# Kernel optimization log

Measured on AMD Instinct MI355X. Metric: run time of the kernel, lower is better.

Reference implementation:

```python
import jax, jax.numpy as jnp
import numpy as np

D, H, L, E, K, FF, VIS, NC, NT = 1024, 8, 4, 4, 2, 2048, 1536, 4, 4
HD = D // H


def layer_norm(x, g, b, eps=1e-5):
    m = x.mean(-1, keepdims=True)
    v = ((x - m) ** 2).mean(-1, keepdims=True)
    return (x - m) / jnp.sqrt(v + eps) * g + b


def sinusoidal_pos(seq_len):
    pos = jnp.arange(seq_len, dtype=jnp.float32)[:, None]
    div = jnp.exp(jnp.arange(0, D, 2, dtype=jnp.float32) * (-jnp.log(10000.0) / D))
    pe = jnp.zeros((seq_len, D), dtype=jnp.float32)
    pe = pe.at[:, 0::2].set(jnp.sin(pos * div))
    pe = pe.at[:, 1::2].set(jnp.cos(pos * div))
    return pe


def mha(x, wi, bi, wo, bo):
    # wi: [D, 3D] (pre-transposed), wo: [D, D]
    B, S, _ = x.shape
    qkv = x @ wi + bi
    q, k, v = jnp.split(qkv, 3, axis=-1)
    split = lambda t: t.reshape(B, S, H, HD).transpose(0, 2, 1, 3)
    q, k, v = split(q), split(k), split(v)
    scores = jnp.einsum('bhqd,bhkd->bhqk', q, k) / jnp.sqrt(jnp.float32(HD))
    a = jax.nn.softmax(scores, axis=-1)
    o = jnp.einsum('bhqk,bhkd->bhqd', a, v).transpose(0, 2, 1, 3).reshape(B, S, D)
    return o @ wo + bo


def moe(x_flat, rw, rb, w1, b1, w2, b2):
    # x_flat: [N, D]; rw: [D, E]; w1: [E, D, FF]; w2: [E, FF, D]
    logits = x_flat @ rw + rb                      # [N, E]
    topv, topi = jax.lax.top_k(logits, K)          # [N, K]
    probs = jax.nn.softmax(topv, axis=-1)          # softmax over the top-k logits
    onehot = jax.nn.one_hot(topi, E, dtype=x_flat.dtype)      # [N, K, E]
    combine = jnp.einsum('nk,nke->ne', probs, onehot)         # [N, E]
    h = jax.nn.relu(jnp.einsum('nd,edf->enf', x_flat, w1) + b1[:, None, :])  # [E, N, FF]
    o = jnp.einsum('enf,efd->end', h, w2) + b2[:, None, :]                   # [E, N, D]
    return jnp.einsum('ne,end->nd', combine, o)


def setup_inputs() -> dict:
    key = jax.random.key(0)
    ks = iter(jax.random.split(key, 32))
    s = 0.02
    n = lambda shape: jax.random.normal(next(ks), shape, dtype=jnp.float32) * s
    inp = {
        'vis_feat': jax.random.normal(next(ks), (64, 128, VIS), dtype=jnp.float32),
        'proj_w': n((VIS, D)), 'proj_b': jnp.zeros((D,), jnp.float32),
        'in_proj_w': n((L, D, 3 * D)), 'in_proj_b': jnp.zeros((L, 3 * D), jnp.float32),
        'out_proj_w': n((L, D, D)), 'out_proj_b': jnp.zeros((L, D), jnp.float32),
        'ln1_g': jnp.ones((L, D), jnp.float32), 'ln1_b': jnp.zeros((L, D), jnp.float32),
        'ln2_g': jnp.ones((L, D), jnp.float32), 'ln2_b': jnp.zeros((L, D), jnp.float32),
        'router_w': n((L, D, E)), 'router_b': jnp.zeros((L, E), jnp.float32),
        'ew1': n((L, E, D, FF)), 'eb1': jnp.zeros((L, E, FF), jnp.float32),
        'ew2': n((L, E, FF, D)), 'eb2': jnp.zeros((L, E, D), jnp.float32),
        'attn_w': n((D, 1)), 'attn_b': jnp.zeros((1,), jnp.float32),
        'heads_w': n((NT, D, NC)), 'heads_b': jnp.zeros((NT, NC), jnp.float32),
    }
    return inp


def reference(vis_feat, proj_w, proj_b, in_proj_w, in_proj_b, out_proj_w, out_proj_b,
              ln1_g, ln1_b, ln2_g, ln2_b, router_w, router_b, ew1, eb1, ew2, eb2,
              attn_w, attn_b, heads_w, heads_b):
    B, S, _ = vis_feat.shape
    x = vis_feat @ proj_w + proj_b            # projection to d_model=1024
    x = x + sinusoidal_pos(S)[None]           # positional encoding
    for l in range(L):                         # 4 MoE transformer layers
        x = layer_norm(x + mha(x, in_proj_w[l], in_proj_b[l], out_proj_w[l], out_proj_b[l]),
                       ln1_g[l], ln1_b[l])
        moe_out = moe(x.reshape(B * S, D), router_w[l], router_b[l],
                      ew1[l], eb1[l], ew2[l], eb2[l]).reshape(B, S, D)
        x = layer_norm(x + moe_out, ln2_g[l], ln2_b[l])
    # attention pooling over time, then 4 task heads
    scores = jax.nn.softmax(x @ attn_w + attn_b, axis=1)   # [B, S, 1]
    pooled = jnp.sum(scores * x, axis=1)                   # [B, D]
    logits = jnp.einsum('bd,tdc->tbc', pooled, heads_w) + heads_b[:, None, :]  # [4, B, 4]
    return logits
```

## Files before the change

kernel.cpp:

```cpp
#include <hip/hip_runtime.h>
#include <hip/hip_bf16.h>

typedef unsigned short u16;
typedef unsigned int u32;
using short8 = __attribute__((ext_vector_type(8))) short;
using f32x4  = __attribute__((ext_vector_type(4))) float;

__device__ __forceinline__ u16 f2bu(float f) {
  u32 u = __builtin_bit_cast(u32, f);
  u32 r = u + 0x7fffu + ((u >> 16) & 1u);
  return (u16)(r >> 16);
}
__device__ __forceinline__ float bu2f(u16 u) {
  u32 x = ((u32)u) << 16;
  return __builtin_bit_cast(float, x);
}
__device__ __forceinline__ float waveRedSum(float v) {
  #pragma unroll
  for (int off = 32; off > 0; off >>= 1) v += __shfl_xor(v, off, 64);
  return v;
}
__device__ __forceinline__ void gload16(const void* g, void* l) {
  __builtin_amdgcn_global_load_lds((const __attribute__((address_space(1))) u32*)g,
                                   (__attribute__((address_space(3))) u32*)l, 16, 0, 0);
}

template<int MODE>
__global__ __launch_bounds__(256) void gemm_bt(
    const u16* __restrict__ A, const u16* __restrict__ Bt, const float* __restrict__ bias,
    float* __restrict__ Cf, u16* __restrict__ Cb, u16* __restrict__ M0, u16* __restrict__ M1,
    const int* __restrict__ tok, const float* __restrict__ prob, const int* __restrict__ slot,
    const int* __restrict__ poff, const int* __restrict__ cnts,
    int N, int K)
{
  const int gx = gridDim.x;
  const int nwg = gx * gridDim.y;
  int lid = blockIdx.y * gx + blockIdx.x;
  lid = (lid & 7) * (nwg >> 3) + (lid >> 3);
  const int brow = (lid / gx) << 7, bcol = (lid % gx) << 7;

  int e = 0, rowEnd = 0;
  const u16* Bw = Bt;
  const float* bw = bias;
  if constexpr (MODE >= 2) {
    if (brow >= poff[4]) return;
    #pragma unroll
    for (int q = 1; q < 4; ++q) if (brow >= poff[q]) e = q;
    rowEnd = poff[e] + cnts[e];
    Bw = Bt + (size_t)e * N * K;
    bw = bias + e * N;
  }

  __shared__ __align__(16) u16 As[128 * 64];
  __shared__ __align__(16) u16 Bs[128 * 64];
  const int tid = threadIdx.x;
  const int wave = tid >> 6, lane = tid & 63;
  const int wr = wave >> 1, wc = wave & 1;
  const int r = lane & 15, kg = lane >> 4;

  f32x4 acc[4][4];
  #pragma unroll
  for (int m = 0; m < 4; ++m)
    #pragma unroll
    for (int n = 0; n < 4; ++n) acc[m][n] = f32x4{0.f, 0.f, 0.f, 0.f};

  const u16* aSrc[4];
  const u16* bSrc[4];
  const u16* Bb = Bw + (size_t)bcol * K;
  #pragma unroll
  for (int q = 0; q < 4; ++q) {
    const int cid = (q << 8) + (wave << 6) + lane;
    const int row = cid >> 3, c = cid & 7;
    const int scol = (c ^ (row & 7)) << 3;
    size_t ar;
    if constexpr (MODE == 2) {
      const int g = brow + row;
      ar = (size_t)tok[(g < rowEnd) ? g : poff[e]];
    } else {
      ar = (size_t)(brow + row);
    }
    aSrc[q] = A + ar * K + scol;
    bSrc[q] = Bb + (size_t)row * K + scol;
  }
  const int swz0 = (kg ^ (r & 7)) << 3;
  const int swz1 = ((4 + kg) ^ (r & 7)) << 3;

  for (int k0 = 0; k0 < K; k0 += 64) {
    __syncthreads();
    #pragma unroll
    for (int q = 0; q < 4; ++q) {
      gload16(aSrc[q] + k0, &As[(((q << 8) + (wave << 6))) << 3]);
      gload16(bSrc[q] + k0, &Bs[(((q << 8) + (wave << 6))) << 3]);
    }
    __syncthreads();
    #pragma unroll
    for (int ks = 0; ks < 2; ++ks) {
      const int swz = ks ? swz1 : swz0;
      short8 a[4], b[4];
      #pragma unroll
      for (int m = 0; m < 4; ++m)
        a[m] = *(const short8*)&As[(((wr << 6) + (m << 4) + r) << 6) + swz];
      #pragma unroll
      for (int n = 0; n < 4; ++n)
        b[n] = *(const short8*)&Bs[(((wc << 6) + (n << 4) + r) << 6) + swz];
      #pragma unroll
      for (int m = 0; m < 4; ++m)
        #pragma unroll
        for (int n = 0; n < 4; ++n)
          acc[m][n] = __builtin_amdgcn_mfma_f32_16x16x32_bf16(a[m], b[n], acc[m][n], 0, 0, 0);
    }
  }

  if constexpr (MODE == 3) {
    #pragma unroll
    for (int m = 0; m < 4; ++m) {
      #pragma unroll
      for (int i4 = 0; i4 < 4; ++i4) {
        const int row = brow + (wr << 6) + (m << 4) + (kg << 2) + i4;
        if (row < rowEnd) {
          const int t = tok[row];
          const float pp = prob[row];
          u16* dst = slot[row] ? M1 : M0;
          #pragma unroll
          for (int n = 0; n < 4; ++n) {
            const int col = bcol + (wc << 6) + (n << 4) + r;
            dst[(size_t)t * N + col] = f2bu((acc[m][n][i4] + bw[col]) * pp);
          }
        }
      }
    }
  } else {
    #pragma unroll
    for (int m = 0; m < 4; ++m) {
      #pragma unroll
      for (int n = 0; n < 4; ++n) {
        const int col = bcol + (wc << 6) + (n << 4) + r;
        const float bv = bw[col];
        #pragma unroll
        for (int i4 = 0; i4 < 4; ++i4) {
          const int row = brow + (wr << 6) + (m << 4) + (kg << 2) + i4;
          const float v = acc[m][n][i4] + bv;
          const size_t off = (size_t)row * N + col;
          if constexpr (MODE == 0) Cf[off] = v;
          else if constexpr (MODE == 1) Cb[off] = f2bu(v);
          else Cb[off] = f2bu(fmaxf(v, 0.f));
        }
      }
    }
  }
}

__device__ __forceinline__ void tconv_tile(const float* __restrict__ s, u16* __restrict__ d,
                                           int K, int N, int n0, int k0)
{
  __shared__ float t[32][33];
  const int x = threadIdx.x, y = threadIdx.y;
  #pragma unroll
  for (int j = 0; j < 4; ++j) t[y + 8 * j][x] = s[(size_t)(k0 + y + 8 * j) * N + n0 + x];
  __syncthreads();
  #pragma unroll
  for (int j = 0; j < 4; ++j) d[(size_t)(n0 + y + 8 * j) * K + k0 + x] = f2bu(t[x][y + 8 * j]);
}

__global__ __launch_bounds__(256) void tconv_kernel(const float* __restrict__ src, u16* __restrict__ dst,
                                                    int K, int N)
{
  tconv_tile(src, dst, K, N, blockIdx.x << 5, blockIdx.y << 5);
}

__global__ __launch_bounds__(256) void tconv4_kernel(
    const float* __restrict__ wqkv_s, const float* __restrict__ wout_s,
    const float* __restrict__ we1_s, const float* __restrict__ we2_s,
    u16* __restrict__ wqkv_d, u16* __restrict__ wout_d,
    u16* __restrict__ we1_d, u16* __restrict__ we2_d)
{
  const int bid = blockIdx.x;
  if (bid < 3072) {
    tconv_tile(wqkv_s, wqkv_d, 1024, 3072, (bid % 96) << 5, (bid / 96) << 5);
  } else if (bid < 4096) {
    const int b2 = bid - 3072;
    tconv_tile(wout_s, wout_d, 1024, 1024, (b2 % 32) << 5, (b2 / 32) << 5);
  } else if (bid < 12288) {
    const int b2 = bid - 4096;
    const int ee = b2 >> 11, rr = b2 & 2047;
    tconv_tile(we1_s + (size_t)ee * 2048 * 1024, we1_d + (size_t)ee * 2048 * 1024,
               1024, 2048, (rr % 64) << 5, (rr / 64) << 5);
  } else {
    const int b2 = bid - 12288;
    const int ee = b2 >> 11, rr = b2 & 2047;
    tconv_tile(we2_s + (size_t)ee * 1024 * 2048, we2_d + (size_t)ee * 1024 * 2048,
               2048, 1024, (rr % 32) << 5, (rr / 32) << 5);
  }
}

__global__ __launch_bounds__(256) void conv_kernel(const float* __restrict__ in, u16* __restrict__ out)
{
  const size_t i = ((size_t)blockIdx.x * 256 + threadIdx.x) * 4;
  float4 v = *(const float4*)(in + i);
  *(ushort4*)(out + i) = make_ushort4(f2bu(v.x), f2bu(v.y), f2bu(v.z), f2bu(v.w));
}

__global__ __launch_bounds__(256) void pe_kernel(float* __restrict__ X, u16* __restrict__ Xb)
{
  const int idx = blockIdx.x * 256 + threadIdx.x;
  const int d = idx & 1023;
  const int s = (idx >> 10) & 127;
  const float de = (float)(d & ~1);
  const float ang = (float)s * expf(de * (-9.210340371976184f / 1024.f));
  const float pe = (d & 1) ? cosf(ang) : sinf(ang);
  const float v = X[idx] + pe;
  X[idx] = v;
  Xb[idx] = f2bu(v);
}

__global__ __launch_bounds__(256) void ln_kernel(const float* __restrict__ Xi, const u16* __restrict__ R,
    const float* __restrict__ g, const float* __restrict__ be,
    const float* __restrict__ rw, const float* __restrict__ rb,
    float* __restrict__ Xo, u16* __restrict__ Xbo,
    int* __restrict__ choice, float* __restrict__ prob2)
{
  const int token = blockIdx.x;
  const size_t base = (size_t)token << 10;
  const int tid = threadIdx.x;
  float vals[4]; float s = 0.f, s2 = 0.f;
  #pragma unroll
  for (int j = 0; j < 4; ++j) {
    const int d = tid + (j << 8);
    const float v = Xi[base + d] + bu2f(R[base + d]);
    vals[j] = v; s += v; s2 += v * v;
  }
  s = waveRedSum(s); s2 = waveRedSum(s2);
  __shared__ float rs[4], rs2[4];
  __shared__ float rl[4][4];
  const int wave = tid >> 6, lane = tid & 63;
  if (lane == 0) { rs[wave] = s; rs2[wave] = s2; }
  __syncthreads();
  s = rs[0] + rs[1] + rs[2] + rs[3];
  s2 = rs2[0] + rs2[1] + rs2[2] + rs2[3];
  const float mean = s * (1.f / 1024.f);
  const float var = s2 * (1.f / 1024.f) - mean * mean;
  const float inv = rsqrtf(var + 1e-5f);
  float l0 = 0.f, l1 = 0.f, l2 = 0.f, l3 = 0.f;
  #pragma unroll
  for (int j = 0; j < 4; ++j) {
    const int d = tid + (j << 8);
    const float y = (vals[j] - mean) * inv * g[d] + be[d];
    Xo[base + d] = y;
    Xbo[base + d] = f2bu(y);
    const float4 w = *(const float4*)(rw + ((size_t)d << 2));
    l0 += y * w.x; l1 += y * w.y; l2 += y * w.z; l3 += y * w.w;
  }
  l0 = waveRedSum(l0); l1 = waveRedSum(l1); l2 = waveRedSum(l2); l3 = waveRedSum(l3);
  if (lane == 0) { rl[wave][0] = l0; rl[wave][1] = l1; rl[wave][2] = l2; rl[wave][3] = l3; }
  __syncthreads();
  if (tid == 0) {
    float v[4];
    #pragma unroll
    for (int q = 0; q < 4; ++q)
      v[q] = rl[0][q] + rl[1][q] + rl[2][q] + rl[3][q] + rb[q];
    int i1 = 0;
    for (int q = 1; q < 4; ++q) if (v[q] > v[i1]) i1 = q;
    int i2 = (i1 == 0) ? 1 : 0;
    for (int q = 0; q < 4; ++q) if (q != i1 && v[q] > v[i2]) i2 = q;
    const float p2 = __expf(v[i2] - v[i1]);
    const float is = 1.f / (1.f + p2);
    choice[token] = i1 | (i2 << 8);
    prob2[token * 2]     = is;
    prob2[token * 2 + 1] = p2 * is;
  }
}

__global__ __launch_bounds__(256) void ln2_kernel(const float* __restrict__ Xi,
    const u16* __restrict__ R0, const u16* __restrict__ R1,
    const float* __restrict__ g, const float* __restrict__ be,
    float* __restrict__ Xo, u16* __restrict__ Xbo,
    const float* __restrict__ aw, const float* __restrict__ ab, float* __restrict__ S)
{
  const int token = blockIdx.x;
  const size_t base = (size_t)token << 10;
  const int tid = threadIdx.x;
  float vals[4]; float s = 0.f, s2 = 0.f;
  #pragma unroll
  for (int j = 0; j < 4; ++j) {
    const int d = tid + (j << 8);
    const float v = Xi[base + d] + (bu2f(R0[base + d]) + bu2f(R1[base + d]));
    vals[j] = v; s += v; s2 += v * v;
  }
  s = waveRedSum(s); s2 = waveRedSum(s2);
  __shared__ float rs[4], rs2[4];
  __shared__ float rsc[4];
  const int wave = tid >> 6, lane = tid & 63;
  if (lane == 0) { rs[wave] = s; rs2[wave] = s2; }
  __syncthreads();
  s = rs[0] + rs[1] + rs[2] + rs[3];
  s2 = rs2[0] + rs2[1] + rs2[2] + rs2[3];
  const float mean = s * (1.f / 1024.f);
  const float var = s2 * (1.f / 1024.f) - mean * mean;
  const float inv = rsqrtf(var + 1e-5f);
  float sc = 0.f;
  #pragma unroll
  for (int j = 0; j < 4; ++j) {
    const int d = tid + (j << 8);
    const float y = (vals[j] - mean) * inv * g[d] + be[d];
    Xo[base + d] = y;
    Xbo[base + d] = f2bu(y);
    if (aw) sc += y * aw[d];
  }
  if (aw) {
    sc = waveRedSum(sc);
    if (lane == 0) rsc[wave] = sc;
    __syncthreads();
    if (tid == 0) S[token] = rsc[0] + rsc[1] + rsc[2] + rsc[3] + ab[0];
  }
}

#define LDW 136
__global__ __launch_bounds__(256) void attn_mfma_kernel(const u16* __restrict__ QKVb, u16* __restrict__ ATTb)
{
  __shared__ __align__(16) u16 Kb[128 * LDW];
  __shared__ __align__(16) u16 Vt[128 * LDW];
  u16* Pb = Kb;
  const int b = blockIdx.x >> 3, h = blockIdx.x & 7;
  const int tid = threadIdx.x;
  const int wave = tid >> 6, lane = tid & 63;
  const int r = lane & 15, kg = lane >> 4;
  const u16* base = QKVb + (size_t)b * 128 * 3072 + h * 128;

  for (int i = tid; i < 128 * 16; i += 256) {
    const int row = i >> 4, c8 = (i & 15) << 3;
    *(short8*)&Kb[row * LDW + c8] = *(const short8*)(base + (size_t)row * 3072 + 1024 + c8);
  }
  for (int i = tid; i < 128 * 128; i += 256) {
    const int d = i & 127, key = i >> 7;
    Vt[d * LDW + key] = base[(size_t)key * 3072 + 2048 + d];
  }

  short8 a[2][4];
  #pragma unroll
  for (int m = 0; m < 2; ++m) {
    const int row = wave * 32 + m * 16 + r;
    const u16* qp = base + (size_t)row * 3072;
    #pragma unroll
    for (int ks = 0; ks < 4; ++ks)
      a[m][ks] = *(const short8*)(qp + ks * 32 + kg * 8);
  }
  __syncthreads();

  f32x4 acc[2][8];
  #pragma unroll
  for (int m = 0; m < 2; ++m)
    #pragma unroll
    for (int n = 0; n < 8; ++n) acc[m][n] = f32x4{0.f, 0.f, 0.f, 0.f};
  #pragma unroll
  for (int n = 0; n < 8; ++n) {
    #pragma unroll
    for (int ks = 0; ks < 4; ++ks) {
      short8 bf = *(const short8*)&Kb[(n * 16 + r) * LDW + ks * 32 + kg * 8];
      #pragma unroll
      for (int m = 0; m < 2; ++m)
        acc[m][n] = __builtin_amdgcn_mfma_f32_16x16x32_bf16(a[m][ks], bf, acc[m][n], 0, 0, 0);
    }
  }
  __syncthreads();

  const float sc = 0.08838834764831845f;
  #pragma unroll
  for (int m = 0; m < 2; ++m) {
    #pragma unroll
    for (int i = 0; i < 4; ++i) {
      float mx = -1e30f;
      #pragma unroll
      for (int n = 0; n < 8; ++n) mx = fmaxf(mx, acc[m][n][i]);
      #pragma unroll
      for (int msk = 1; msk < 16; msk <<= 1) mx = fmaxf(mx, __shfl_xor(mx, msk, 64));
      float s = 0.f;
      #pragma unroll
      for (int n = 0; n < 8; ++n) { float pv = __expf((acc[m][n][i] - mx) * sc); acc[m][n][i] = pv; s += pv; }
      #pragma unroll
      for (int msk = 1; msk < 16; msk <<= 1) s += __shfl_xor(s, msk, 64);
      const float inv = 1.f / s;
      #pragma unroll
      for (int n = 0; n < 8; ++n) {
        const int prow = wave * 32 + m * 16 + kg * 4 + i;
        Pb[prow * LDW + n * 16 + r] = f2bu(acc[m][n][i] * inv);
      }
    }
  }

  f32x4 oacc[2][8];
  #pragma unroll
  for (int m = 0; m < 2; ++m)
    #pragma unroll
    for (int n = 0; n < 8; ++n) oacc[m][n] = f32x4{0.f, 0.f, 0.f, 0.f};
  #pragma unroll
  for (int ks = 0; ks < 4; ++ks) {
    short8 pa[2];
    #pragma unroll
    for (int m = 0; m < 2; ++m)
      pa[m] = *(const short8*)&Pb[(wave * 32 + m * 16 + r) * LDW + ks * 32 + kg * 8];
    #pragma unroll
    for (int n = 0; n < 8; ++n) {
      short8 vb = *(const short8*)&Vt[(n * 16 + r) * LDW + ks * 32 + kg * 8];
      #pragma unroll
      for (int m = 0; m < 2; ++m)
        oacc[m][n] = __builtin_amdgcn_mfma_f32_16x16x32_bf16(pa[m], vb, oacc[m][n], 0, 0, 0);
    }
  }

  u16* op = ATTb + ((size_t)b * 128) * 1024 + h * 128;
  #pragma unroll
  for (int m = 0; m < 2; ++m) {
    #pragma unroll
    for (int n = 0; n < 8; ++n) {
      #pragma unroll
      for (int i = 0; i < 4; ++i) {
        const int row = wave * 32 + m * 16 + kg * 4 + i;
        op[(size_t)row * 1024 + n * 16 + r] = f2bu(oacc[m][n][i]);
      }
    }
  }
}
#undef LDW

__global__ __launch_bounds__(256) void build_lists_kernel(
    const int* __restrict__ choice, const float* __restrict__ prob2,
    int* __restrict__ cnt, int* __restrict__ poff,
    int* __restrict__ tok, float* __restrict__ prob, int* __restrict__ slot)
{
  const int tid = threadIdx.x;
  const int e = tid >> 6, lane = tid & 63;
  const int t0 = lane << 7;
  int mycount = 0;
  for (int j = 0; j < 128; ++j) {
    const int c = choice[t0 + j];
    mycount += (((c & 255) == e) || ((c >> 8) == e)) ? 1 : 0;
  }
  int incl = mycount;
  #pragma unroll
  for (int off = 1; off < 64; off <<= 1) {
    const int t = __shfl_up(incl, off, 64);
    if (lane >= off) incl += t;
  }
  __shared__ int totals[4];
  if (lane == 63) totals[e] = incl;
  __syncthreads();
  int base = 0;
  #pragma unroll
  for (int q = 0; q < 4; ++q)
    if (q < e) base += (totals[q] + 255) & ~255;
  int pos = base + incl - mycount;
  for (int j = 0; j < 128; ++j) {
    const int token = t0 + j;
    const int c = choice[token];
    const int m = ((c & 255) == e) ? 1 : (((c >> 8) == e) ? 2 : 0);
    if (m) {
      tok[pos] = token;
      prob[pos] = prob2[token * 2 + (m - 1)];
      slot[pos] = m - 1;
      ++pos;
    }
  }
  if (lane == 0) {
    cnt[e] = totals[e];
    poff[e] = base;
    if (e == 3) poff[4] = base + ((totals[3] + 255) & ~255);
  }
}

__global__ __launch_bounds__(256) void pool_kernel(const float* __restrict__ X, const float* __restrict__ S,
                                                   float* __restrict__ P)
{
  const int b = blockIdx.x;
  const int tid = threadIdx.x;
  __shared__ float p[128];
  if (tid < 128) p[tid] = S[b * 128 + tid];
  __syncthreads();
  float mx = -1e30f;
  for (int t = 0; t < 128; ++t) mx = fmaxf(mx, p[t]);
  float sum = 0.f;
  for (int t = 0; t < 128; ++t) sum += __expf(p[t] - mx);
  const float inv = 1.f / sum;
  __syncthreads();
  if (tid < 128) p[tid] = __expf(p[tid] - mx) * inv;
  __syncthreads();
  float acc[4] = {0.f, 0.f, 0.f, 0.f};
  for (int t = 0; t < 128; ++t) {
    const float pt = p[t];
    const float* xp = X + ((size_t)(b * 128 + t) << 10) + tid;
    #pragma unroll
    for (int j = 0; j < 4; ++j) acc[j] += pt * xp[j << 8];
  }
  #pragma unroll
  for (int j = 0; j < 4; ++j) P[((size_t)b << 10) + tid + (j << 8)] = acc[j];
}

__global__ __launch_bounds__(256) void heads_kernel(const float* __restrict__ P, const float* __restrict__ hw,
    const float* __restrict__ hb, float* __restrict__ out)
{
  const int idx = blockIdx.x * 4 + (threadIdx.x >> 6);
  const int lane = threadIdx.x & 63;
  const int t = idx >> 8, b = (idx >> 2) & 63, c = idx & 3;
  const float* pp = P + ((size_t)b << 10);
  const float* wp = hw + (size_t)t * 4096 + c;
  float s = 0.f;
  #pragma unroll
  for (int j = 0; j < 16; ++j) { const int k = lane + (j << 6); s += pp[k] * wp[(size_t)k << 2]; }
  s = waveRedSum(s);
  if (lane == 0) out[idx] = s + hb[t * 4 + c];
}

extern "C" void kernel_launch(void* const* d_in, const int* in_sizes, int n_in,
                              void* d_out, int out_size, void* d_ws, size_t ws_size,
                              hipStream_t stream)
{
  (void)in_sizes; (void)n_in; (void)out_size; (void)ws_size;
  const float* vis        = (const float*)d_in[0];
  const float* proj_w     = (const float*)d_in[1];
  const float* proj_b     = (const float*)d_in[2];
  const float* in_proj_w  = (const float*)d_in[3];
  const float* in_proj_b  = (const float*)d_in[4];
  const float* out_proj_w = (const float*)d_in[5];
  const float* out_proj_b = (const float*)d_in[6];
  const float* ln1_g      = (const float*)d_in[7];
  const float* ln1_b      = (const float*)d_in[8];
  const float* ln2_g      = (const float*)d_in[9];
  const float* ln2_b      = (const float*)d_in[10];
  const float* router_w   = (const float*)d_in[11];
  const float* router_b   = (const float*)d_in[12];
  const float* ew1        = (const float*)d_in[13];
  const float* eb1        = (const float*)d_in[14];
  const float* ew2        = (const float*)d_in[15];
  const float* eb2        = (const float*)d_in[16];
  const float* attn_w     = (const float*)d_in[17];
  const float* attn_b     = (const float*)d_in[18];
  const float* heads_w    = (const float*)d_in[19];
  const float* heads_b    = (const float*)d_in[20];
  float* out = (float*)d_out;

  char* p = (char*)d_ws;
  auto take = [&](size_t bytes) -> char* {
    char* q = p; p += (bytes + 255) & ~(size_t)255; return q;
  };
  float* X    = (float*)take(8192ULL * 1024 * 4);
  u16*   Xb   = (u16*)  take(8192ULL * 1024 * 2);
  char*  QKVr = take(104857600ULL);
  u16*   ATTb = (u16*)  take(8192ULL * 1024 * 2);
  int*   CNT  = (int*)  take(4 * 4);
  int*   POFF = (int*)  take(5 * 4);
  int*   CHOICE = (int*)take(8192ULL * 4);
  float* PROB2  = (float*)take(8192ULL * 2 * 4);
  int*   TOK  = (int*)  take(17408ULL * 4);
  float* PROB = (float*)take(17408ULL * 4);
  int*   SLOT = (int*)  take(17408ULL * 4);
  float* S    = (float*)take(8192ULL * 4);
  float* POOL = (float*)take(64ULL * 1024 * 4);
  u16*   Wqkv = (u16*)  take(3072ULL * 1024 * 2);
  u16*   Wout = (u16*)  take(1024ULL * 1024 * 2);
  u16*   We1  = (u16*)  take(4ULL * 2048 * 1024 * 2);
  u16*   We2  = (u16*)  take(4ULL * 1024 * 2048 * 2);
  u16*   QKVb  = (u16*)QKVr;
  u16*   O16   = (u16*)QKVr;
  u16*   H     = (u16*)QKVr;
  u16*   MOE0b = (u16*)(QKVr + 71303168);
  u16*   MOE1b = (u16*)(QKVr + 71303168 + 16777216);
  u16*   Wproj = We1;
  u16*   VISb  = (u16*)QKVr;

  const dim3 tb(32, 8);
  #define GARGS Cf_, Cb_, MOE0b, MOE1b, TOK, PROB, SLOT, POFF, CNT

  tconv_kernel<<<dim3(1024 / 32, 1536 / 32), tb, 0, stream>>>(proj_w, Wproj, 1536, 1024);
  conv_kernel<<<(8192 * 1536 / 4) / 256, 256, 0, stream>>>(vis, VISb);
  {
    float* Cf_ = X; u16* Cb_ = nullptr;
    gemm_bt<0><<<dim3(8, 64), 256, 0, stream>>>(VISb, Wproj, proj_b, GARGS, 1024, 1536);
  }
  pe_kernel<<<8192 * 1024 / 256, 256, 0, stream>>>(X, Xb);

  for (int l = 0; l < 4; ++l) {
    tconv4_kernel<<<20480, tb, 0, stream>>>(
        in_proj_w + (size_t)l * 1024 * 3072, out_proj_w + (size_t)l * 1024 * 1024,
        ew1 + (size_t)l * 4 * 1024 * 2048, ew2 + (size_t)l * 4 * 2048 * 1024,
        Wqkv, Wout, We1, We2);

    {
      float* Cf_ = nullptr; u16* Cb_ = QKVb;
      gemm_bt<1><<<dim3(24, 64), 256, 0, stream>>>(Xb, Wqkv, in_proj_b + l * 3072, GARGS, 3072, 1024);
    }
    attn_mfma_kernel<<<512, 256, 0, stream>>>(QKVb, ATTb);
    {
      float* Cf_ = nullptr; u16* Cb_ = O16;
      gemm_bt<1><<<dim3(8, 64), 256, 0, stream>>>(ATTb, Wout, out_proj_b + l * 1024, GARGS, 1024, 1024);
    }
    ln_kernel<<<8192, 256, 0, stream>>>(X, O16, ln1_g + l * 1024, ln1_b + l * 1024,
                                        router_w + (size_t)l * 4096, router_b + l * 4,
                                        X, Xb, CHOICE, PROB2);
    build_lists_kernel<<<1, 256, 0, stream>>>(CHOICE, PROB2, CNT, POFF, TOK, PROB, SLOT);
    {
      float* Cf_ = nullptr; u16* Cb_ = H;
      gemm_bt<2><<<dim3(16, 136), 256, 0, stream>>>(Xb, We1, eb1 + (size_t)l * 4 * 2048, GARGS, 2048, 1024);
    }
    {
      float* Cf_ = nullptr; u16* Cb_ = nullptr;
      gemm_bt<3><<<dim3(8, 136), 256, 0, stream>>>(H, We2, eb2 + (size_t)l * 4 * 1024, GARGS, 1024, 2048);
    }
    ln2_kernel<<<8192, 256, 0, stream>>>(X, MOE0b, MOE1b, ln2_g + l * 1024, ln2_b + l * 1024,
                                         X, Xb, (l == 3) ? attn_w : nullptr, attn_b, S);
  }

  pool_kernel<<<64, 256, 0, stream>>>(X, S, POOL);
  heads_kernel<<<256, 256, 0, stream>>>(POOL, heads_w, heads_b, out);
  #undef GARGS
}
```

Before: 1.844 ms.

## Drop fp32 residual stream; keep activations only in bf16 and vectorize LN

```diff
diff --git a/kernel.cpp b/kernel.cpp
--- a/kernel.cpp
+++ b/kernel.cpp
@@ -200,35 +200,40 @@
   *(ushort4*)(out + i) = make_ushort4(f2bu(v.x), f2bu(v.y), f2bu(v.z), f2bu(v.w));
 }
 
-__global__ __launch_bounds__(256) void pe_kernel(float* __restrict__ X, u16* __restrict__ Xb)
-{
-  const int idx = blockIdx.x * 256 + threadIdx.x;
-  const int d = idx & 1023;
+__global__ __launch_bounds__(256) void pe_kernel(u16* __restrict__ Xb)
+{
+  const int idx = (blockIdx.x * 256 + threadIdx.x) * 4;
   const int s = (idx >> 10) & 127;
-  const float de = (float)(d & ~1);
-  const float ang = (float)s * expf(de * (-9.210340371976184f / 1024.f));
-  const float pe = (d & 1) ? cosf(ang) : sinf(ang);
-  const float v = X[idx] + pe;
-  X[idx] = v;
-  Xb[idx] = f2bu(v);
-}
-
-__global__ __launch_bounds__(256) void ln_kernel(const float* __restrict__ Xi, const u16* __restrict__ R,
+  ushort4 v = *(const ushort4*)(Xb + idx);
+  float o[4];
+  const u16 vv[4] = {v.x, v.y, v.z, v.w};
+  #pragma unroll
+  for (int j = 0; j < 4; ++j) {
+    const int d = (idx + j) & 1023;
+    const float de = (float)(d & ~1);
+    const float ang = (float)s * expf(de * (-9.210340371976184f / 1024.f));
+    const float pe = (d & 1) ? cosf(ang) : sinf(ang);
+    o[j] = bu2f(vv[j]) + pe;
+  }
+  *(ushort4*)(Xb + idx) = make_ushort4(f2bu(o[0]), f2bu(o[1]), f2bu(o[2]), f2bu(o[3]));
+}
+
+__global__ __launch_bounds__(256) void ln_kernel(u16* __restrict__ Xb, const u16* __restrict__ R,
     const float* __restrict__ g, const float* __restrict__ be,
     const float* __restrict__ rw, const float* __restrict__ rb,
-    float* __restrict__ Xo, u16* __restrict__ Xbo,
     int* __restrict__ choice, float* __restrict__ prob2)
 {
   const int token = blockIdx.x;
   const size_t base = (size_t)token << 10;
   const int tid = threadIdx.x;
-  float vals[4]; float s = 0.f, s2 = 0.f;
-  #pragma unroll
-  for (int j = 0; j < 4; ++j) {
-    const int d = tid + (j << 8);
-    const float v = Xi[base + d] + bu2f(R[base + d]);
-    vals[j] = v; s += v; s2 += v * v;
-  }
+  const int d0 = tid << 2;
+  ushort4 xv = *(const ushort4*)(Xb + base + d0);
+  ushort4 rv = *(const ushort4*)(R + base + d0);
+  float vals[4] = {bu2f(xv.x) + bu2f(rv.x), bu2f(xv.y) + bu2f(rv.y),
+                   bu2f(xv.z) + bu2f(rv.z), bu2f(xv.w) + bu2f(rv.w)};
+  float s = 0.f, s2 = 0.f;
+  #pragma unroll
+  for (int j = 0; j < 4; ++j) { s += vals[j]; s2 += vals[j] * vals[j]; }
   s = waveRedSum(s); s2 = waveRedSum(s2);
   __shared__ float rs[4], rs2[4];
   __shared__ float rl[4][4];
@@ -240,15 +245,19 @@
   const float mean = s * (1.f / 1024.f);
   const float var = s2 * (1.f / 1024.f) - mean * mean;
   const float inv = rsqrtf(var + 1e-5f);
+  const float4 gv = *(const float4*)(g + d0);
+  const float4 bv = *(const float4*)(be + d0);
+  float y[4];
+  y[0] = (vals[0] - mean) * inv * gv.x + bv.x;
+  y[1] = (vals[1] - mean) * inv * gv.y + bv.y;
+  y[2] = (vals[2] - mean) * inv * gv.z + bv.z;
+  y[3] = (vals[3] - mean) * inv * gv.w + bv.w;
+  *(ushort4*)(Xb + base + d0) = make_ushort4(f2bu(y[0]), f2bu(y[1]), f2bu(y[2]), f2bu(y[3]));
   float l0 = 0.f, l1 = 0.f, l2 = 0.f, l3 = 0.f;
   #pragma unroll
   for (int j = 0; j < 4; ++j) {
-    const int d = tid + (j << 8);
-    const float y = (vals[j] - mean) * inv * g[d] + be[d];
-    Xo[base + d] = y;
-    Xbo[base + d] = f2bu(y);
-    const float4 w = *(const float4*)(rw + ((size_t)d << 2));
-    l0 += y * w.x; l1 += y * w.y; l2 += y * w.z; l3 += y * w.w;
+    const float4 w = *(const float4*)(rw + ((size_t)(d0 + j) << 2));
+    l0 += y[j] * w.x; l1 += y[j] * w.y; l2 += y[j] * w.z; l3 += y[j] * w.w;
   }
   l0 = waveRedSum(l0); l1 = waveRedSum(l1); l2 = waveRedSum(l2); l3 = waveRedSum(l3);
   if (lane == 0) { rl[wave][0] = l0; rl[wave][1] = l1; rl[wave][2] = l2; rl[wave][3] = l3; }
@@ -270,22 +279,25 @@
   }
 }
 
-__global__ __launch_bounds__(256) void ln2_kernel(const float* __restrict__ Xi,
+__global__ __launch_bounds__(256) void ln2_kernel(u16* __restrict__ Xb,
     const u16* __restrict__ R0, const u16* __restrict__ R1,
     const float* __restrict__ g, const float* __restrict__ be,
-    float* __restrict__ Xo, u16* __restrict__ Xbo,
     const float* __restrict__ aw, const float* __restrict__ ab, float* __restrict__ S)
 {
   const int token = blockIdx.x;
   const size_t base = (size_t)token << 10;
   const int tid = threadIdx.x;
-  float vals[4]; float s = 0.f, s2 = 0.f;
-  #pragma unroll
-  for (int j = 0; j < 4; ++j) {
-    const int d = tid + (j << 8);
-    const float v = Xi[base + d] + (bu2f(R0[base + d]) + bu2f(R1[base + d]));
-    vals[j] = v; s += v; s2 += v * v;
-  }
+  const int d0 = tid << 2;
+  ushort4 xv = *(const ushort4*)(Xb + base + d0);
+  ushort4 r0 = *(const ushort4*)(R0 + base + d0);
+  ushort4 r1 = *(const ushort4*)(R1 + base + d0);
+  float vals[4] = {bu2f(xv.x) + (bu2f(r0.x) + bu2f(r1.x)),
+                   bu2f(xv.y) + (bu2f(r0.y) + bu2f(r1.y)),
+                   bu2f(xv.z) + (bu2f(r0.z) + bu2f(r1.z)),
+                   bu2f(xv.w) + (bu2f(r0.w) + bu2f(r1.w))};
+  float s = 0.f, s2 = 0.f;
+  #pragma unroll
+  for (int j = 0; j < 4; ++j) { s += vals[j]; s2 += vals[j] * vals[j]; }
   s = waveRedSum(s); s2 = waveRedSum(s2);
   __shared__ float rs[4], rs2[4];
   __shared__ float rsc[4];
@@ -297,16 +309,17 @@
   const float mean = s * (1.f / 1024.f);
   const float var = s2 * (1.f / 1024.f) - mean * mean;
   const float inv = rsqrtf(var + 1e-5f);
-  float sc = 0.f;
-  #pragma unroll
-  for (int j = 0; j < 4; ++j) {
-    const int d = tid + (j << 8);
-    const float y = (vals[j] - mean) * inv * g[d] + be[d];
-    Xo[base + d] = y;
-    Xbo[base + d] = f2bu(y);
-    if (aw) sc += y * aw[d];
-  }
+  const float4 gv = *(const float4*)(g + d0);
+  const float4 bv = *(const float4*)(be + d0);
+  float y[4];
+  y[0] = (vals[0] - mean) * inv * gv.x + bv.x;
+  y[1] = (vals[1] - mean) * inv * gv.y + bv.y;
+  y[2] = (vals[2] - mean) * inv * gv.z + bv.z;
+  y[3] = (vals[3] - mean) * inv * gv.w + bv.w;
+  *(ushort4*)(Xb + base + d0) = make_ushort4(f2bu(y[0]), f2bu(y[1]), f2bu(y[2]), f2bu(y[3]));
   if (aw) {
+    const float4 av = *(const float4*)(aw + d0);
+    float sc = y[0] * av.x + y[1] * av.y + y[2] * av.z + y[3] * av.w;
     sc = waveRedSum(sc);
     if (lane == 0) rsc[wave] = sc;
     __syncthreads();
@@ -467,7 +480,7 @@
   }
 }
 
-__global__ __launch_bounds__(256) void pool_kernel(const float* __restrict__ X, const float* __restrict__ S,
+__global__ __launch_bounds__(256) void pool_kernel(const u16* __restrict__ Xb, const float* __restrict__ S,
                                                    float* __restrict__ P)
 {
   const int b = blockIdx.x;
@@ -486,9 +499,9 @@
   float acc[4] = {0.f, 0.f, 0.f, 0.f};
   for (int t = 0; t < 128; ++t) {
     const float pt = p[t];
-    const float* xp = X + ((size_t)(b * 128 + t) << 10) + tid;
-    #pragma unroll
-    for (int j = 0; j < 4; ++j) acc[j] += pt * xp[j << 8];
+    const u16* xp = Xb + ((size_t)(b * 128 + t) << 10) + tid;
+    #pragma unroll
+    for (int j = 0; j < 4; ++j) acc[j] += pt * bu2f(xp[j << 8]);
   }
   #pragma unroll
   for (int j = 0; j < 4; ++j) P[((size_t)b << 10) + tid + (j << 8)] = acc[j];
@@ -541,7 +554,6 @@
   auto take = [&](size_t bytes) -> char* {
     char* q = p; p += (bytes + 255) & ~(size_t)255; return q;
   };
-  float* X    = (float*)take(8192ULL * 1024 * 4);
   u16*   Xb   = (u16*)  take(8192ULL * 1024 * 2);
   char*  QKVr = take(104857600ULL);
   u16*   ATTb = (u16*)  take(8192ULL * 1024 * 2);
@@ -572,10 +584,10 @@
   tconv_kernel<<<dim3(1024 / 32, 1536 / 32), tb, 0, stream>>>(proj_w, Wproj, 1536, 1024);
   conv_kernel<<<(8192 * 1536 / 4) / 256, 256, 0, stream>>>(vis, VISb);
   {
-    float* Cf_ = X; u16* Cb_ = nullptr;
-    gemm_bt<0><<<dim3(8, 64), 256, 0, stream>>>(VISb, Wproj, proj_b, GARGS, 1024, 1536);
-  }
-  pe_kernel<<<8192 * 1024 / 256, 256, 0, stream>>>(X, Xb);
+    float* Cf_ = nullptr; u16* Cb_ = Xb;
+    gemm_bt<1><<<dim3(8, 64), 256, 0, stream>>>(VISb, Wproj, proj_b, GARGS, 1024, 1536);
+  }
+  pe_kernel<<<8192 * 1024 / 4 / 256, 256, 0, stream>>>(Xb);
 
   for (int l = 0; l < 4; ++l) {
     tconv4_kernel<<<20480, tb, 0, stream>>>(
@@ -592,9 +604,9 @@
       float* Cf_ = nullptr; u16* Cb_ = O16;
       gemm_bt<1><<<dim3(8, 64), 256, 0, stream>>>(ATTb, Wout, out_proj_b + l * 1024, GARGS, 1024, 1024);
     }
-    ln_kernel<<<8192, 256, 0, stream>>>(X, O16, ln1_g + l * 1024, ln1_b + l * 1024,
+    ln_kernel<<<8192, 256, 0, stream>>>(Xb, O16, ln1_g + l * 1024, ln1_b + l * 1024,
                                         router_w + (size_t)l * 4096, router_b + l * 4,
-                                        X, Xb, CHOICE, PROB2);
+                                        CHOICE, PROB2);
     build_lists_kernel<<<1, 256, 0, stream>>>(CHOICE, PROB2, CNT, POFF, TOK, PROB, SLOT);
     {
       float* Cf_ = nullptr; u16* Cb_ = H;
@@ -604,11 +616,11 @@
       float* Cf_ = nullptr; u16* Cb_ = nullptr;
       gemm_bt<3><<<dim3(8, 136), 256, 0, stream>>>(H, We2, eb2 + (size_t)l * 4 * 1024, GARGS, 1024, 2048);
     }
-    ln2_kernel<<<8192, 256, 0, stream>>>(X, MOE0b, MOE1b, ln2_g + l * 1024, ln2_b + l * 1024,
-                                         X, Xb, (l == 3) ? attn_w : nullptr, attn_b, S);
-  }
-
-  pool_kernel<<<64, 256, 0, stream>>>(X, S, POOL);
+    ln2_kernel<<<8192, 256, 0, stream>>>(Xb, MOE0b, MOE1b, ln2_g + l * 1024, ln2_b + l * 1024,
+                                         (l == 3) ? attn_w : nullptr, attn_b, S);
+  }
+
+  pool_kernel<<<64, 256, 0, stream>>>(Xb, S, POOL);
   heads_kernel<<<256, 256, 0, stream>>>(POOL, heads_w, heads_b, out);
   #undef GARGS
 }
```

Result: faster. 1.804 ms (-2.2%).
